# Performance work log

Measured on AMD Instinct MI355X. Metric: run time of the kernel, lower is better.

The kernel has to match this reference:

```python
import jax, jax.numpy as jnp
import numpy as np
import math

# Config: 8 packed images, each a 32x32 patch grid (t=1) -> equal seglen 1024
NSEG, GH, GW = 8, 32, 32
L = GH * GW            # 1024 tokens per segment
S = NSEG * L           # 8192 packed tokens
H, NH = 1024, 16
HD = H // NH           # 64, head dim (rope dim), divisible by 4
MLP = 4096
THETA = 10000.0


def _make_rope_cos_sin():
    # Rope2DPosEmb._precompute_freqs_cis for a (GH, GW) grid, dim=HD
    flat = np.arange(L, dtype=np.float32)
    x_pos = flat % GW
    y_pos = flat // GW
    dim_range = np.arange(0, HD, 4, dtype=np.float32)[: HD // 4]
    freqs = 1.0 / THETA ** (dim_range / HD)          # [HD//4]
    x_f = np.outer(x_pos, freqs)                     # [L, HD//4]
    y_f = np.outer(y_pos, freqs)
    # interleave x/y angles per frequency -> [L, HD//2]
    ang = np.stack([x_f, y_f], axis=-1).reshape(L, HD // 2)
    ang = np.tile(ang, (NSEG, 1))                    # same grid repeated per image
    return jnp.asarray(np.cos(ang)), jnp.asarray(np.sin(ang))


def setup_inputs() -> dict:
    key = jax.random.key(0)
    ks = jax.random.split(key, 8)
    cos, sin = _make_rope_cos_sin()
    inp = {
        "x": jax.random.normal(ks[0], (S, H), jnp.float32),
        "wqkv": jax.random.normal(ks[1], (3 * H, H), jnp.float32) * math.sqrt(1.0 / H),
        "wo": jax.random.normal(ks[2], (H, H), jnp.float32) * math.sqrt(1.0 / H),
        "ln0_g": jnp.ones((H,), jnp.float32),
        "ln0_b": jnp.zeros((H,), jnp.float32),
        "ln1_g": jnp.ones((H,), jnp.float32),
        "ln1_b": jnp.zeros((H,), jnp.float32),
        "fc0_w": jax.random.normal(ks[3], (MLP, H), jnp.float32) * math.sqrt(2.0 / H),
        "fc0_b": jnp.zeros((MLP,), jnp.float32),
        "fc1_w": jax.random.normal(ks[4], (H, MLP), jnp.float32) * math.sqrt(2.0 / MLP),
        "fc1_b": jnp.zeros((H,), jnp.float32),
        "rope_cos": cos,
        "rope_sin": sin,
        "cu_seqlens": jnp.arange(NSEG + 1, dtype=jnp.int32) * L,
    }
    return inp


def _layernorm(x, g, b, eps=1e-5):
    m = x.mean(-1, keepdims=True)
    v = ((x - m) ** 2).mean(-1, keepdims=True)
    return (x - m) * jax.lax.rsqrt(v + eps) * g + b


def _apply_rope(x, cos, sin):
    # x: [S, NH, HD]; cos/sin: [S, HD//2]. Complex mult on (even, odd) pairs.
    xr = x.reshape(S, NH, HD // 2, 2)
    x0, x1 = xr[..., 0], xr[..., 1]
    c = cos[:, None, :]
    s = sin[:, None, :]
    o0 = x0 * c - x1 * s
    o1 = x0 * s + x1 * c
    return jnp.stack([o0, o1], axis=-1).reshape(S, NH, HD)


def reference(x, wqkv, wo, ln0_g, ln0_b, ln1_g, ln1_b,
              fc0_w, fc0_b, fc1_w, fc1_b, rope_cos, rope_sin, cu_seqlens):
    # --- attention branch (pre-norm) ---
    h = _layernorm(x, ln0_g, ln0_b)
    qkv = (h @ wqkv.T).reshape(S, 3, NH, HD)
    q, k, v = qkv[:, 0], qkv[:, 1], qkv[:, 2]
    q = _apply_rope(q, rope_cos, rope_sin)
    k = _apply_rope(k, rope_cos, rope_sin)
    # block-diagonal varlen attention: equal-length segments -> reshape
    qb = q.reshape(NSEG, L, NH, HD)
    kb = k.reshape(NSEG, L, NH, HD)
    vb = v.reshape(NSEG, L, NH, HD)
    scores = jnp.einsum("blhd,bmhd->bhlm", qb, kb) / math.sqrt(HD)
    p = jax.nn.softmax(scores.astype(jnp.float32), axis=-1).astype(x.dtype)
    attn = jnp.einsum("bhlm,bmhd->blhd", p, vb).reshape(S, H)
    x = x + attn @ wo.T
    # --- MLP branch (pre-norm) ---
    h2 = _layernorm(x, ln1_g, ln1_b)
    mlp = jax.nn.gelu(h2 @ fc0_w.T + fc0_b, approximate=False) @ fc1_w.T + fc1_b
    return x + mlp
```

## Files before the change

### kernel.cpp

```cpp
#include <hip/hip_runtime.h>
#include <math.h>


typedef __bf16 bf16x8 __attribute__((ext_vector_type(8)));
typedef float f32x4 __attribute__((ext_vector_type(4)));
typedef float f32x16 __attribute__((ext_vector_type(16)));
typedef unsigned int u32;

__device__ __forceinline__ unsigned short f2b(float f) {
  unsigned u = __float_as_uint(f);
  return (unsigned short)((u + 0x7FFFu + ((u >> 16) & 1u)) >> 16);
}
__device__ __forceinline__ float b2f(unsigned short h) {
  return __uint_as_float(((unsigned)h) << 16);
}
__device__ __forceinline__ void async_ld16(const void* g, void* l) {
  __builtin_amdgcn_global_load_lds((__attribute__((address_space(1))) void*)g,
                                   (__attribute__((address_space(3))) void*)l,
                                   16, 0, 0);
}
__device__ __forceinline__ float exp2fast(float x) {
#if __has_builtin(__builtin_amdgcn_exp2f)
  return __builtin_amdgcn_exp2f(x);
#else
  return exp2f(x);
#endif
}
__device__ __forceinline__ float rcpfast(float x) {
#if __has_builtin(__builtin_amdgcn_rcpf)
  return __builtin_amdgcn_rcpf(x);
#else
  return 1.0f / x;
#endif
}

__global__ __launch_bounds__(256) void castln_kernel(
    const float* __restrict__ w0, const float* __restrict__ w1,
    const float* __restrict__ w2, const float* __restrict__ w3,
    unsigned short* __restrict__ wdst,
    const float* __restrict__ x, const float* __restrict__ g,
    const float* __restrict__ bt, unsigned short* __restrict__ hout) {
  __shared__ float red[8];
  const int blk = blockIdx.x;
  if (blk < 12288) {
    const int t = blk * 256 + threadIdx.x;
    const float* src;
    int off;
    if (t < 786432) { src = w0; off = t; }
    else if (t < 1048576) { src = w1; off = t - 786432; }
    else if (t < 2097152) { src = w2; off = t - 1048576; }
    else { src = w3; off = t - 2097152; }
    const float4 v = ((const float4*)src)[off];
    ushort4 o;
    o.x = f2b(v.x); o.y = f2b(v.y); o.z = f2b(v.z); o.w = f2b(v.w);
    ((ushort4*)wdst)[t] = o;
    return;
  }
  const int row = blk - 12288, t = threadIdx.x;
  const float4 v = ((const float4*)(x + (size_t)row * 1024))[t];
  float s = v.x + v.y + v.z + v.w;
  float s2 = v.x * v.x + v.y * v.y + v.z * v.z + v.w * v.w;
#pragma unroll
  for (int m = 1; m < 64; m <<= 1) {
    s += __shfl_xor(s, m, 64);
    s2 += __shfl_xor(s2, m, 64);
  }
  if ((t & 63) == 0) { red[t >> 6] = s; red[4 + (t >> 6)] = s2; }
  __syncthreads();
  const float ts = red[0] + red[1] + red[2] + red[3];
  const float ts2 = red[4] + red[5] + red[6] + red[7];
  const float mean = ts * (1.f / 1024.f);
  const float var = ts2 * (1.f / 1024.f) - mean * mean;
  const float inv = rsqrtf(var + 1e-5f);
  const float4 gv = ((const float4*)g)[t];
  const float4 bv = ((const float4*)bt)[t];
  ushort4 o;
  o.x = f2b((v.x - mean) * inv * gv.x + bv.x);
  o.y = f2b((v.y - mean) * inv * gv.y + bv.y);
  o.z = f2b((v.z - mean) * inv * gv.z + bv.z);
  o.w = f2b((v.w - mean) * inv * gv.w + bv.w);
  ((ushort4*)hout)[(size_t)row * 256 + t] = o;
}

__global__ __launch_bounds__(256) void ln_kernel(const float* __restrict__ x,
                                                 const float* __restrict__ g,
                                                 const float* __restrict__ bt,
                                                 unsigned short* __restrict__ out) {
  __shared__ float red[8];
  const int row = blockIdx.x, t = threadIdx.x;
  const float4 v = ((const float4*)(x + (size_t)row * 1024))[t];
  float s = v.x + v.y + v.z + v.w;
  float s2 = v.x * v.x + v.y * v.y + v.z * v.z + v.w * v.w;
#pragma unroll
  for (int m = 1; m < 64; m <<= 1) {
    s += __shfl_xor(s, m, 64);
    s2 += __shfl_xor(s2, m, 64);
  }
  if ((t & 63) == 0) { red[t >> 6] = s; red[4 + (t >> 6)] = s2; }
  __syncthreads();
  const float ts = red[0] + red[1] + red[2] + red[3];
  const float ts2 = red[4] + red[5] + red[6] + red[7];
  const float mean = ts * (1.f / 1024.f);
  const float var = ts2 * (1.f / 1024.f) - mean * mean;
  const float inv = rsqrtf(var + 1e-5f);
  const float4 gv = ((const float4*)g)[t];
  const float4 bv = ((const float4*)bt)[t];
  ushort4 o;
  o.x = f2b((v.x - mean) * inv * gv.x + bv.x);
  o.y = f2b((v.y - mean) * inv * gv.y + bv.y);
  o.z = f2b((v.z - mean) * inv * gv.z + bv.z);
  o.w = f2b((v.w - mean) * inv * gv.w + bv.w);
  ((ushort4*)out)[(size_t)row * 256 + t] = o;
}

template <int MODE, int NBN>
__global__ __launch_bounds__(256) void gemm_bt(
    const unsigned short* __restrict__ A, const unsigned short* __restrict__ B,
    int M, int N, int K, float* __restrict__ outf, unsigned short* __restrict__ outb,
    const float* __restrict__ res, const float* __restrict__ bias) {
  __shared__ __align__(16) unsigned short As[128 * 32];
  __shared__ __align__(16) unsigned short Bs[128 * 32];
  const int bid = blockIdx.x;
  const int j8 = bid & 7, g = bid >> 3;
  const int bm = ((g / NBN) * 8 + j8) * 128;
  const int bn = (g % NBN) * 128;
  const int t = threadIdx.x, wave = t >> 6, lane = t & 63;
  const int quad = lane >> 4, l16 = lane & 15;
  const int wm = (wave >> 1) * 64, wn = (wave & 1) * 64;
  const int srow = lane >> 2;
  const int scol = (((lane & 3) ^ ((lane >> 3) & 3)) * 8);
  const unsigned short* Ag0 = A + (size_t)(bm + wave * 32 + srow) * K + scol;
  const unsigned short* Ag1 = Ag0 + (size_t)16 * K;
  const unsigned short* Bg0 = B + (size_t)(bn + wave * 32 + srow) * K + scol;
  const unsigned short* Bg1 = Bg0 + (size_t)16 * K;
  unsigned short* Al = As + wave * 1024;
  unsigned short* Bl = Bs + wave * 1024;
  const int swg = (l16 >> 1) & 3;
  f32x4 acc[4][4] = {};
  for (int k0 = 0; k0 < K; k0 += 32) {
    async_ld16(Ag0 + k0, Al);
    async_ld16(Ag1 + k0, Al + 512);
    async_ld16(Bg0 + k0, Bl);
    async_ld16(Bg1 + k0, Bl + 512);
    __syncthreads();
    bf16x8 af[4], bfv[4];
#pragma unroll
    for (int i = 0; i < 4; i++)
      af[i] = *(const bf16x8*)(As + (wm + i * 16 + l16) * 32 + (quad ^ swg) * 8);
#pragma unroll
    for (int jj = 0; jj < 4; jj++)
      bfv[jj] = *(const bf16x8*)(Bs + (wn + jj * 16 + l16) * 32 + (quad ^ swg) * 8);
#pragma unroll
    for (int i = 0; i < 4; i++)
#pragma unroll
      for (int jj = 0; jj < 4; jj++)
        acc[i][jj] = __builtin_amdgcn_mfma_f32_16x16x32_bf16(af[i], bfv[jj], acc[i][jj], 0, 0, 0);
    __syncthreads();
  }
#pragma unroll
  for (int i = 0; i < 4; i++)
#pragma unroll
    for (int jj = 0; jj < 4; jj++)
#pragma unroll
      for (int r = 0; r < 4; r++) {
        const int m = bm + wm + i * 16 + quad * 4 + r;
        const int n = bn + wn + jj * 16 + l16;
        const size_t idx = (size_t)m * N + n;
        const float v = acc[i][jj][r];
        if (MODE == 1) {
          outf[idx] = v + res[idx];
        } else if (MODE == 2) {
          const float z = v + bias[n];
          const float u = z * (0.7978845608f + 0.03567740814f * z * z);
          const float e = fminf(u * 2.885390082f, 80.f);
          const float tt = exp2fast(e);
          outb[idx] = f2b(z * tt * rcpfast(tt + 1.0f));
        } else if (MODE == 3) {
          outf[idx] = v + bias[n] + res[idx];
        } else {
          outb[idx] = f2b(v);
        }
      }
}

__device__ __forceinline__ u32 rope2(u32 in, float c, float sn, float sc) {
  const float a = b2f((unsigned short)(in & 0xffff));
  const float b = b2f((unsigned short)(in >> 16));
  return (u32)f2b((a * c - b * sn) * sc) | ((u32)f2b((a * sn + b * c) * sc) << 16);
}
__global__ __launch_bounds__(256) void ropevt_kernel(const unsigned short* __restrict__ qkv,
                                                     const float* __restrict__ cb,
                                                     const float* __restrict__ sb,
                                                     unsigned short* __restrict__ qh,
                                                     unsigned short* __restrict__ kh,
                                                     unsigned short* __restrict__ vt) {
  __shared__ unsigned short tile[64][72];
  const int blk = blockIdx.x;
  if (blk < 4096) {
    const int tid = blk * 256 + threadIdx.x;
    const int ii = tid & 7, head = (tid >> 3) & 15, s = tid >> 7;
    const float4 cv = *(const float4*)(cb + s * 32 + ii * 4);
    const float4 sv = *(const float4*)(sb + s * 32 + ii * 4);
    const unsigned short* base = qkv + (size_t)s * 3072 + head * 64 + ii * 8;
    const uint4 qa = *(const uint4*)base;
    const uint4 ka = *(const uint4*)(base + 1024);
    const int seg = s >> 10, l = s & 1023;
    const size_t o = ((size_t)((seg * 16 + head) * 1024 + l)) * 64 + ii * 8;
    const float QSC = 0.125f * 1.44269504f;
    uint4 qo, ko;
    qo.x = rope2(qa.x, cv.x, sv.x, QSC); ko.x = rope2(ka.x, cv.x, sv.x, 1.f);
    qo.y = rope2(qa.y, cv.y, sv.y, QSC); ko.y = rope2(ka.y, cv.y, sv.y, 1.f);
    qo.z = rope2(qa.z, cv.z, sv.z, QSC); ko.z = rope2(ka.z, cv.z, sv.z, 1.f);
    qo.w = rope2(qa.w, cv.w, sv.w, QSC); ko.w = rope2(ka.w, cv.w, sv.w, 1.f);
    *(uint4*)(qh + o) = qo;
    *(uint4*)(kh + o) = ko;
    return;
  }
  const int b = blk - 4096;
  const int lt = b & 15, head = (b >> 4) & 15, seg = b >> 8;
  const int t = threadIdx.x;
  const int r = t >> 2, c0 = (t & 3) * 16;
  const unsigned short* src =
      qkv + ((size_t)(seg * 1024 + lt * 64 + r)) * 3072 + 2048 + head * 64 + c0;
#pragma unroll
  for (int k = 0; k < 16; k++) tile[r][c0 + k] = src[k];
  __syncthreads();
  unsigned short* dst =
      vt + ((size_t)((seg * 16 + head) * 64 + r)) * 1024 + lt * 64 + c0;
#pragma unroll
  for (int k = 0; k < 16; k++) dst[k] = tile[c0 + k][r];
}

__global__ __launch_bounds__(256) void attn_kernel(const unsigned short* __restrict__ qh,
                                                   const unsigned short* __restrict__ kh,
                                                   const unsigned short* __restrict__ vt,
                                                   unsigned short* __restrict__ out) {
  __shared__ __align__(16) unsigned short Qs[128 * 64];
  __shared__ __align__(16) unsigned short Ks[64 * 64];
  __shared__ __align__(16) unsigned short Vs[64 * 64];
  __shared__ float wl[128];
  const int b = blockIdx.x;
  const int head = b & 15, seg = (b >> 4) & 7, qt = b >> 7;
  const int t = threadIdx.x, wave = t >> 6, lane = t & 63;
  const int h = lane >> 5, q31 = lane & 31;
  const size_t sh = (size_t)(seg * 16 + head);
  const unsigned short* qbase = qh + (sh * 1024 + (size_t)qt * 128) * 64;
  const unsigned short* kbase = kh + sh * 1024 * 64;
  const unsigned short* vbase = vt + sh * 64 * 1024;
  const int r8 = lane >> 3;
  const int c8 = ((lane & 7) ^ (r8 & 7)) * 8;
#pragma unroll
  for (int cc = 0; cc < 4; cc++) {
    const int chunk = wave * 4 + cc;
    async_ld16(qbase + (size_t)(chunk * 8 + r8) * 64 + c8, Qs + chunk * 512);
  }
  const int qrow_l = wave * 32 + q31;
  const int qsw = qrow_l & 7;
  bf16x8 qf[4];
  float lsum = 0.f;
  f32x16 oacc[2] = {};

  for (int kt = 0; kt < 16; kt++) {
    const int ch0 = wave * 2;
    async_ld16(kbase + (size_t)(kt * 64 + ch0 * 8 + r8) * 64 + c8, Ks + ch0 * 512);
    async_ld16(kbase + (size_t)(kt * 64 + ch0 * 8 + 8 + r8) * 64 + c8, Ks + ch0 * 512 + 512);
    async_ld16(vbase + (size_t)(ch0 * 8 + r8) * 1024 + kt * 64 + c8, Vs + ch0 * 512);
    async_ld16(vbase + (size_t)(ch0 * 8 + 8 + r8) * 1024 + kt * 64 + c8, Vs + ch0 * 512 + 512);
    __syncthreads();
    if (kt == 0) {
#pragma unroll
      for (int ks = 0; ks < 4; ks++)
        qf[ks] = *(const bf16x8*)(Qs + qrow_l * 64 + (((2 * ks + h) ^ qsw)) * 8);
    }
    f32x16 st[2] = {{}, {}};
#pragma unroll
    for (int T = 0; T < 2; T++) {
      const int krow = 32 * T + q31;
      const int ksw = krow & 7;
#pragma unroll
      for (int ks = 0; ks < 4; ks++) {
        const bf16x8 kf = *(const bf16x8*)(Ks + krow * 64 + (((2 * ks + h) ^ ksw)) * 8);
        st[T] = __builtin_amdgcn_mfma_f32_32x32x16_bf16(kf, qf[ks], st[T], 0, 0, 0);
      }
    }
    u32 pk[2][4][2];
#pragma unroll
    for (int T = 0; T < 2; T++)
#pragma unroll
      for (int g = 0; g < 4; g++)
#pragma unroll
        for (int e = 0; e < 2; e++) {
          const float plo = exp2fast(st[T][4 * g + 2 * e]);
          const float phi = exp2fast(st[T][4 * g + 2 * e + 1]);
          lsum += plo + phi;
          pk[T][g][e] = (u32)f2b(plo) | ((u32)f2b(phi) << 16);
        }
    u32 rcv[2][4];
#pragma unroll
    for (int T = 0; T < 2; T++) {
      const u32 p0 = h ? pk[T][0][0] : pk[T][1][0];
      const u32 p1 = h ? pk[T][0][1] : pk[T][1][1];
      const u32 p2 = h ? pk[T][2][0] : pk[T][3][0];
      const u32 p3 = h ? pk[T][2][1] : pk[T][3][1];
      rcv[T][0] = (u32)__shfl_xor((int)p0, 32, 64);
      rcv[T][1] = (u32)__shfl_xor((int)p1, 32, 64);
      rcv[T][2] = (u32)__shfl_xor((int)p2, 32, 64);
      rcv[T][3] = (u32)__shfl_xor((int)p3, 32, 64);
    }
#pragma unroll
    for (int tt = 0; tt < 4; tt++) {
      const int T = tt >> 1, uu = tt & 1;
      union { u32 u[4]; bf16x8 v; } af;
      if (h == 0) {
        af.u[0] = pk[T][2 * uu][0];
        af.u[1] = pk[T][2 * uu][1];
        af.u[2] = rcv[T][2 * uu];
        af.u[3] = rcv[T][2 * uu + 1];
      } else {
        af.u[0] = rcv[T][2 * uu];
        af.u[1] = rcv[T][2 * uu + 1];
        af.u[2] = pk[T][2 * uu + 1][0];
        af.u[3] = pk[T][2 * uu + 1][1];
      }
#pragma unroll
      for (int ot = 0; ot < 2; ot++) {
        const int vrow = 32 * ot + q31;
        const int vsw = vrow & 7;
        const bf16x8 bv = *(const bf16x8*)(Vs + vrow * 64 + (((2 * tt + h) ^ vsw)) * 8);
        oacc[ot] = __builtin_amdgcn_mfma_f32_32x32x16_bf16(af.v, bv, oacc[ot], 0, 0, 0);
      }
    }
    __syncthreads();
  }
  lsum += __shfl_xor(lsum, 32, 64);
  if (h == 0) wl[wave * 32 + q31] = lsum;
  const int qglob = seg * 1024 + qt * 128 + wave * 32;
#pragma unroll
  for (int g = 0; g < 4; g++) {
    const float4 lv = *(const float4*)&wl[wave * 32 + 8 * g + 4 * h];
#pragma unroll
    for (int m = 0; m < 4; m++) {
      const int r16 = 4 * g + m;
      const int qrow = qglob + m + 8 * g + 4 * h;
      const float invl = rcpfast((&lv.x)[m]);
#pragma unroll
      for (int ot = 0; ot < 2; ot++)
        out[(size_t)qrow * 1024 + head * 64 + 32 * ot + q31] = f2b(oacc[ot][r16] * invl);
    }
  }
}

extern "C" void kernel_launch(void* const* d_in, const int* in_sizes, int n_in,
                              void* d_out, int out_size, void* d_ws, size_t ws_size,
                              hipStream_t stream) {
  (void)in_sizes; (void)n_in; (void)out_size; (void)ws_size;
  const float* x    = (const float*)d_in[0];
  const float* wqkv = (const float*)d_in[1];
  const float* wo   = (const float*)d_in[2];
  const float* ln0g = (const float*)d_in[3];
  const float* ln0b = (const float*)d_in[4];
  const float* ln1g = (const float*)d_in[5];
  const float* ln1b = (const float*)d_in[6];
  const float* fc0w = (const float*)d_in[7];
  const float* fc0b = (const float*)d_in[8];
  const float* fc1w = (const float*)d_in[9];
  const float* fc1b = (const float*)d_in[10];
  const float* rc   = (const float*)d_in[11];
  const float* rsn  = (const float*)d_in[12];
  float* out = (float*)d_out;
  char* w = (char*)d_ws;
  const size_t MB = 1u << 20;
  unsigned short* hb    = (unsigned short*)(w + 0);
  unsigned short* bqkv  = (unsigned short*)(w + 16 * MB);
  unsigned short* bwo   = (unsigned short*)(w + 22 * MB);
  unsigned short* bfc0  = (unsigned short*)(w + 24 * MB);
  unsigned short* bfc1  = (unsigned short*)(w + 32 * MB);
  unsigned short* qhb   = (unsigned short*)(w + 40 * MB);
  unsigned short* khb   = (unsigned short*)(w + 56 * MB);
  unsigned short* vtb   = (unsigned short*)(w + 72 * MB);
  unsigned short* attnb = (unsigned short*)(w + 88 * MB);
  unsigned short* qkvb  = (unsigned short*)(w + 104 * MB);
  unsigned short* midb  = (unsigned short*)(w + 104 * MB);

  castln_kernel<<<20480, 256, 0, stream>>>(wqkv, wo, fc0w, fc1w, bqkv,
                                           x, ln0g, ln0b, hb);
  gemm_bt<4, 24><<<1536, 256, 0, stream>>>(hb, bqkv, 8192, 3072, 1024,
                                           nullptr, qkvb, nullptr, nullptr);
  ropevt_kernel<<<6144, 256, 0, stream>>>(qkvb, rc, rsn, qhb, khb, vtb);
  attn_kernel<<<1024, 256, 0, stream>>>(qhb, khb, vtb, attnb);
  gemm_bt<1, 8><<<512, 256, 0, stream>>>(attnb, bwo, 8192, 1024, 1024,
                                         out, nullptr, x, nullptr);
  ln_kernel<<<8192, 256, 0, stream>>>(out, ln1g, ln1b, hb);
  gemm_bt<2, 32><<<2048, 256, 0, stream>>>(hb, bfc0, 8192, 4096, 1024,
                                           nullptr, midb, nullptr, fc0b);
  gemm_bt<3, 8><<<512, 256, 0, stream>>>(midb, bfc1, 8192, 1024, 4096,
                                         out, nullptr, out, fc1b);
}
```

Measured before the change: 526.5 us.

## Double-buffer LDS tiles in GEMM and attention to overlap loads with MFMA

The GEMM kernel now keeps two LDS stages for the A/B tiles and issues the async loads for the next K-step before the current step's MFMAs run. It also replaces the two __syncthreads per iteration with a single vmcnt wait plus barrier, and adds an occupancy hint to launch bounds. The attention kernel applies the same double buffering to its K/V tiles and loads Q fragments straight from global memory into registers, dropping the Q shared-memory tile. The aim is to hide global-to-LDS latency behind compute. In exchange the GEMM LDS footprint doubles, which could limit occupancy.

```diff
diff --git a/kernel.cpp b/kernel.cpp
--- a/kernel.cpp
+++ b/kernel.cpp
@@ -114,12 +114,12 @@
 }
 
 template <int MODE, int NBN>
-__global__ __launch_bounds__(256) void gemm_bt(
+__global__ __launch_bounds__(256, 4) void gemm_ln(
     const unsigned short* __restrict__ A, const unsigned short* __restrict__ B,
     int M, int N, int K, float* __restrict__ outf, unsigned short* __restrict__ outb,
     const float* __restrict__ res, const float* __restrict__ bias) {
-  __shared__ __align__(16) unsigned short As[128 * 32];
-  __shared__ __align__(16) unsigned short Bs[128 * 32];
+  __shared__ __align__(16) unsigned short As[2][128 * 32];
+  __shared__ __align__(16) unsigned short Bs[2][128 * 32];
   const int bid = blockIdx.x;
   const int j8 = bid & 7, g = bid >> 3;
   const int bm = ((g / NBN) * 8 + j8) * 128;
@@ -127,36 +127,58 @@
   const int t = threadIdx.x, wave = t >> 6, lane = t & 63;
   const int quad = lane >> 4, l16 = lane & 15;
   const int wm = (wave >> 1) * 64, wn = (wave & 1) * 64;
-  const int srow = lane >> 2;
-  const int scol = (((lane & 3) ^ ((lane >> 3) & 3)) * 8);
-  const unsigned short* Ag0 = A + (size_t)(bm + wave * 32 + srow) * K + scol;
+  const int r16 = lane >> 2;
+  const int cs8 = (((lane & 3) ^ ((lane >> 3) & 3)) * 8);
+  const unsigned short* Ag0 = A + (size_t)(bm + wave * 32 + r16) * K + cs8;
   const unsigned short* Ag1 = Ag0 + (size_t)16 * K;
-  const unsigned short* Bg0 = B + (size_t)(bn + wave * 32 + srow) * K + scol;
+  const unsigned short* Bg0 = B + (size_t)(bn + wave * 32 + r16) * K + cs8;
   const unsigned short* Bg1 = Bg0 + (size_t)16 * K;
-  unsigned short* Al = As + wave * 1024;
-  unsigned short* Bl = Bs + wave * 1024;
+  unsigned short* Al = &As[0][wave * 1024];
+  unsigned short* Bl = &Bs[0][wave * 1024];
+#define STG(tt, bi)                                                          \
+  do {                                                                       \
+    const size_t ko_ = (size_t)(tt) * 32;                                    \
+    async_ld16(Ag0 + ko_, Al + (bi) * 4096);                                 \
+    async_ld16(Ag1 + ko_, Al + (bi) * 4096 + 512);                           \
+    async_ld16(Bg0 + ko_, Bl + (bi) * 4096);                                 \
+    async_ld16(Bg1 + ko_, Bl + (bi) * 4096 + 512);                           \
+  } while (0)
+
+  f32x4 acc[4][4] = {};
+  const int NT = K >> 5;
   const int swg = (l16 >> 1) & 3;
-  f32x4 acc[4][4] = {};
-  for (int k0 = 0; k0 < K; k0 += 32) {
-    async_ld16(Ag0 + k0, Al);
-    async_ld16(Ag1 + k0, Al + 512);
-    async_ld16(Bg0 + k0, Bl);
-    async_ld16(Bg1 + k0, Bl + 512);
-    __syncthreads();
+  STG(0, 0);
+  asm volatile("s_waitcnt vmcnt(0)" ::: "memory");
+  __builtin_amdgcn_sched_barrier(0);
+  __builtin_amdgcn_s_barrier();
+  __builtin_amdgcn_sched_barrier(0);
+  for (int tt = 0; tt < NT; ++tt) {
+    const int cb = tt & 1;
+    if (tt + 1 < NT) STG(tt + 1, cb ^ 1);
+    const unsigned short* Ab = &As[cb][0];
+    const unsigned short* Bb = &Bs[cb][0];
     bf16x8 af[4], bfv[4];
 #pragma unroll
     for (int i = 0; i < 4; i++)
-      af[i] = *(const bf16x8*)(As + (wm + i * 16 + l16) * 32 + (quad ^ swg) * 8);
-#pragma unroll
-    for (int jj = 0; jj < 4; jj++)
-      bfv[jj] = *(const bf16x8*)(Bs + (wn + jj * 16 + l16) * 32 + (quad ^ swg) * 8);
-#pragma unroll
-    for (int i = 0; i < 4; i++)
-#pragma unroll
-      for (int jj = 0; jj < 4; jj++)
-        acc[i][jj] = __builtin_amdgcn_mfma_f32_16x16x32_bf16(af[i], bfv[jj], acc[i][jj], 0, 0, 0);
-    __syncthreads();
-  }
+      af[i] = *(const bf16x8*)(Ab + (wm + i * 16 + l16) * 32 + (quad ^ swg) * 8);
+#pragma unroll
+    for (int j = 0; j < 4; j++)
+      bfv[j] = *(const bf16x8*)(Bb + (wn + j * 16 + l16) * 32 + (quad ^ swg) * 8);
+#pragma unroll
+    for (int j = 0; j < 4; j++)
+#pragma unroll
+      for (int i = 0; i < 4; i++)
+        acc[i][j] = __builtin_amdgcn_mfma_f32_16x16x32_bf16(af[i], bfv[j],
+                                                            acc[i][j], 0, 0, 0);
+    if (tt + 1 < NT) {
+      __builtin_amdgcn_sched_barrier(0);
+      asm volatile("s_waitcnt vmcnt(0)" ::: "memory");
+      __builtin_amdgcn_sched_barrier(0);
+      __builtin_amdgcn_s_barrier();
+      __builtin_amdgcn_sched_barrier(0);
+    }
+  }
+#undef STG
 #pragma unroll
   for (int i = 0; i < 4; i++)
 #pragma unroll
@@ -173,8 +195,8 @@
           const float z = v + bias[n];
           const float u = z * (0.7978845608f + 0.03567740814f * z * z);
           const float e = fminf(u * 2.885390082f, 80.f);
-          const float tt = exp2fast(e);
-          outb[idx] = f2b(z * tt * rcpfast(tt + 1.0f));
+          const float tt2 = exp2fast(e);
+          outb[idx] = f2b(z * tt2 * rcpfast(tt2 + 1.0f));
         } else if (MODE == 3) {
           outf[idx] = v + bias[n] + res[idx];
         } else {
@@ -235,9 +257,8 @@
                                                    const unsigned short* __restrict__ kh,
                                                    const unsigned short* __restrict__ vt,
                                                    unsigned short* __restrict__ out) {
-  __shared__ __align__(16) unsigned short Qs[128 * 64];
-  __shared__ __align__(16) unsigned short Ks[64 * 64];
-  __shared__ __align__(16) unsigned short Vs[64 * 64];
+  __shared__ __align__(16) unsigned short Ks[2 * 4096];
+  __shared__ __align__(16) unsigned short Vs[2 * 4096];
   __shared__ float wl[128];
   const int b = blockIdx.x;
   const int head = b & 15, seg = (b >> 4) & 7, qt = b >> 7;
@@ -249,29 +270,37 @@
   const unsigned short* vbase = vt + sh * 64 * 1024;
   const int r8 = lane >> 3;
   const int c8 = ((lane & 7) ^ (r8 & 7)) * 8;
-#pragma unroll
-  for (int cc = 0; cc < 4; cc++) {
-    const int chunk = wave * 4 + cc;
-    async_ld16(qbase + (size_t)(chunk * 8 + r8) * 64 + c8, Qs + chunk * 512);
-  }
+  const int ch0 = wave * 2;
+#define STAGEKV(kt, bi)                                                        \
+  do {                                                                         \
+    async_ld16(kbase + (size_t)((kt) * 64 + ch0 * 8 + r8) * 64 + c8,           \
+               Ks + (bi) * 4096 + ch0 * 512);                                  \
+    async_ld16(kbase + (size_t)((kt) * 64 + ch0 * 8 + 8 + r8) * 64 + c8,       \
+               Ks + (bi) * 4096 + ch0 * 512 + 512);                            \
+    async_ld16(vbase + (size_t)(ch0 * 8 + r8) * 1024 + (kt) * 64 + c8,         \
+               Vs + (bi) * 4096 + ch0 * 512);                                  \
+    async_ld16(vbase + (size_t)(ch0 * 8 + 8 + r8) * 1024 + (kt) * 64 + c8,     \
+               Vs + (bi) * 4096 + ch0 * 512 + 512);                            \
+  } while (0)
+
   const int qrow_l = wave * 32 + q31;
-  const int qsw = qrow_l & 7;
   bf16x8 qf[4];
+#pragma unroll
+  for (int ks = 0; ks < 4; ks++)
+    qf[ks] = *(const bf16x8*)(qbase + (size_t)qrow_l * 64 + ks * 16 + h * 8);
+  STAGEKV(0, 0);
+  asm volatile("s_waitcnt vmcnt(0)" ::: "memory");
+  __builtin_amdgcn_sched_barrier(0);
+  __builtin_amdgcn_s_barrier();
+  __builtin_amdgcn_sched_barrier(0);
+
   float lsum = 0.f;
   f32x16 oacc[2] = {};
-
   for (int kt = 0; kt < 16; kt++) {
-    const int ch0 = wave * 2;
-    async_ld16(kbase + (size_t)(kt * 64 + ch0 * 8 + r8) * 64 + c8, Ks + ch0 * 512);
-    async_ld16(kbase + (size_t)(kt * 64 + ch0 * 8 + 8 + r8) * 64 + c8, Ks + ch0 * 512 + 512);
-    async_ld16(vbase + (size_t)(ch0 * 8 + r8) * 1024 + kt * 64 + c8, Vs + ch0 * 512);
-    async_ld16(vbase + (size_t)(ch0 * 8 + 8 + r8) * 1024 + kt * 64 + c8, Vs + ch0 * 512 + 512);
-    __syncthreads();
-    if (kt == 0) {
-#pragma unroll
-      for (int ks = 0; ks < 4; ks++)
-        qf[ks] = *(const bf16x8*)(Qs + qrow_l * 64 + (((2 * ks + h) ^ qsw)) * 8);
-    }
+    const int cbuf = kt & 1;
+    if (kt + 1 < 16) STAGEKV(kt + 1, cbuf ^ 1);
+    const unsigned short* Kb = Ks + cbuf * 4096;
+    const unsigned short* Vb = Vs + cbuf * 4096;
     f32x16 st[2] = {{}, {}};
 #pragma unroll
     for (int T = 0; T < 2; T++) {
@@ -279,7 +308,7 @@
       const int ksw = krow & 7;
 #pragma unroll
       for (int ks = 0; ks < 4; ks++) {
-        const bf16x8 kf = *(const bf16x8*)(Ks + krow * 64 + (((2 * ks + h) ^ ksw)) * 8);
+        const bf16x8 kf = *(const bf16x8*)(Kb + krow * 64 + (((2 * ks + h) ^ ksw)) * 8);
         st[T] = __builtin_amdgcn_mfma_f32_32x32x16_bf16(kf, qf[ks], st[T], 0, 0, 0);
       }
     }
@@ -326,12 +355,19 @@
       for (int ot = 0; ot < 2; ot++) {
         const int vrow = 32 * ot + q31;
         const int vsw = vrow & 7;
-        const bf16x8 bv = *(const bf16x8*)(Vs + vrow * 64 + (((2 * tt + h) ^ vsw)) * 8);
+        const bf16x8 bv = *(const bf16x8*)(Vb + vrow * 64 + (((2 * tt + h) ^ vsw)) * 8);
         oacc[ot] = __builtin_amdgcn_mfma_f32_32x32x16_bf16(af.v, bv, oacc[ot], 0, 0, 0);
       }
     }
-    __syncthreads();
-  }
+    if (kt + 1 < 16) {
+      __builtin_amdgcn_sched_barrier(0);
+      asm volatile("s_waitcnt vmcnt(0)" ::: "memory");
+      __builtin_amdgcn_sched_barrier(0);
+      __builtin_amdgcn_s_barrier();
+      __builtin_amdgcn_sched_barrier(0);
+    }
+  }
+#undef STAGEKV
   lsum += __shfl_xor(lsum, 32, 64);
   if (h == 0) wl[wave * 32 + q31] = lsum;
   const int qglob = seg * 1024 + qt * 128 + wave * 32;
@@ -384,15 +420,15 @@
 
   castln_kernel<<<20480, 256, 0, stream>>>(wqkv, wo, fc0w, fc1w, bqkv,
                                            x, ln0g, ln0b, hb);
-  gemm_bt<4, 24><<<1536, 256, 0, stream>>>(hb, bqkv, 8192, 3072, 1024,
+  gemm_ln<4, 24><<<1536, 256, 0, stream>>>(hb, bqkv, 8192, 3072, 1024,
                                            nullptr, qkvb, nullptr, nullptr);
   ropevt_kernel<<<6144, 256, 0, stream>>>(qkvb, rc, rsn, qhb, khb, vtb);
   attn_kernel<<<1024, 256, 0, stream>>>(qhb, khb, vtb, attnb);
-  gemm_bt<1, 8><<<512, 256, 0, stream>>>(attnb, bwo, 8192, 1024, 1024,
+  gemm_ln<1, 8><<<512, 256, 0, stream>>>(attnb, bwo, 8192, 1024, 1024,
                                          out, nullptr, x, nullptr);
   ln_kernel<<<8192, 256, 0, stream>>>(out, ln1g, ln1b, hb);
-  gemm_bt<2, 32><<<2048, 256, 0, stream>>>(hb, bfc0, 8192, 4096, 1024,
+  gemm_ln<2, 32><<<2048, 256, 0, stream>>>(hb, bfc0, 8192, 4096, 1024,
                                            nullptr, midb, nullptr, fc0b);
-  gemm_bt<3, 8><<<512, 256, 0, stream>>>(midb, bfc1, 8192, 1024, 4096,
+  gemm_ln<3, 8><<<512, 256, 0, stream>>>(midb, bfc1, 8192, 1024, 4096,
                                          out, nullptr, out, fc1b);
 }
```

After: 512.6 us. 2.6% less time.
